# Optimization experiments

Hardware: AMD Instinct MI355X
Metric: run time of the kernel (lower is better)

Reference implementation:

```python
import jax, jax.numpy as jnp
import numpy as np

EMBED_DIM = 768
NUM_HEADS = 12
HEAD_DIM = EMBED_DIM // NUM_HEADS
B, S = 2, 2048


def setup_inputs() -> dict:
    key = jax.random.key(0)
    ks = jax.random.split(key, 6)
    glorot = jnp.sqrt(6.0 / (EMBED_DIM + EMBED_DIM)).astype(jnp.float32)
    x = jax.random.normal(ks[0], (B, S, EMBED_DIM), dtype=jnp.float32)
    mask = jnp.zeros((1, 1, S, S), dtype=jnp.float32)  # additive mask, 0 = no masking
    Wq = jax.random.uniform(ks[1], (EMBED_DIM, EMBED_DIM), jnp.float32, -glorot, glorot)
    Wk = jax.random.uniform(ks[2], (EMBED_DIM, EMBED_DIM), jnp.float32, -glorot, glorot)
    Wv = jax.random.uniform(ks[3], (EMBED_DIM, EMBED_DIM), jnp.float32, -glorot, glorot)
    Wo = jax.random.uniform(ks[4], (EMBED_DIM, EMBED_DIM), jnp.float32, -glorot, glorot)
    bo = jnp.zeros((EMBED_DIM,), dtype=jnp.float32)
    return {"x": x, "mask": mask, "Wq": Wq, "Wk": Wk, "Wv": Wv, "Wo": Wo, "bo": bo}


def reference(x, mask, Wq, Wk, Wv, Wo, bo):
    b, s, _ = x.shape
    # Q/K/V projections (no bias), split into heads: [b, h, s, d]
    def split_heads(t):
        return t.reshape(b, s, NUM_HEADS, HEAD_DIM).transpose(0, 2, 1, 3)
    q = split_heads(x @ Wq)
    k = split_heads(x @ Wk)
    v = split_heads(x @ Wv)
    scale = 1.0 / jnp.sqrt(jnp.float32(HEAD_DIM))
    logits = jnp.einsum('bhqd,bhkd->bhqk', q, k) * scale  # [b, h, s, s]
    logits = logits + mask * (-1e9)
    weights = jax.nn.softmax(logits, axis=-1)
    attn = jnp.einsum('bhqk,bhkd->bhqd', weights, v)
    concat = attn.transpose(0, 2, 1, 3).reshape(b, s, EMBED_DIM)
    return concat @ Wo + bo
```

## Files before the change

kernel.cpp:

```cpp
#include <hip/hip_runtime.h>


typedef __bf16 bf16_t;
typedef bf16_t bf16x8 __attribute__((ext_vector_type(8)));
typedef bf16_t bf16x4 __attribute__((ext_vector_type(4)));
typedef float f32x4 __attribute__((ext_vector_type(4)));
typedef _Float16 f16x4 __attribute__((ext_vector_type(4)));
typedef _Float16 f16x8 __attribute__((ext_vector_type(8)));
typedef __fp16 hf2 __attribute__((ext_vector_type(2)));

#define SC2 0.1803368801111137f
#define DEFER_THR 44.0f

__device__ __forceinline__ float bf2f(unsigned short u) {
  union { unsigned int i; float f; } x;
  x.i = ((unsigned int)u) << 16;
  return x.f;
}

__device__ __forceinline__ float fexp2(float x) {
  return __builtin_amdgcn_exp2f(x);
}

__device__ __forceinline__ void glds16(const bf16_t* g, bf16_t* l) {
  __builtin_amdgcn_global_load_lds(
      (const __attribute__((address_space(1))) void*)g,
      (__attribute__((address_space(3))) void*)l, 16, 0, 0);
}

__device__ __forceinline__ int detect_bf16_flag(const unsigned short* x) {
  const int lane = threadIdx.x & 63;
  const uint4* p = (const uint4*)x;
  uint4 a = p[lane * 2];
  uint4 b = p[lane * 2 + 1];
  unsigned int w[8] = {a.x, a.y, a.z, a.w, b.x, b.y, b.z, b.w};
  unsigned int big = 0;
#pragma unroll
  for (int i = 0; i < 8; i++) {
    unsigned int e0 = (w[i] >> 7) & 0xFF, e1 = (w[i] >> 23) & 0xFF;
    big |= (e0 > 0x88u) | (e1 > 0x88u);
  }
  unsigned long long bal = __ballot(big != 0u);
  return bal == 0ULL ? 1 : 0;
}

__global__ void k_prep(const void* __restrict__ x, const void* __restrict__ mask,
                       const void* __restrict__ Wq, const void* __restrict__ Wk,
                       const void* __restrict__ Wv, const void* __restrict__ Wo,
                       bf16_t* __restrict__ xb, bf16_t* __restrict__ wqkvT,
                       bf16_t* __restrict__ woT, int* __restrict__ mflags) {
  __shared__ float ts[32][33];
  __shared__ int snz;
  const int blk = blockIdx.x;
  const int f = detect_bf16_flag((const unsigned short*)x);

  if (blk < 1536) {
    if (f) return;
    int i = blk * 256 + threadIdx.x;
    const float* xf = (const float*)x + (size_t)i * 8;
    bf16x8 v;
#pragma unroll
    for (int j = 0; j < 8; j++) v[j] = (bf16_t)xf[j];
    *(bf16x8*)(xb + (size_t)i * 8) = v;
  } else if (blk < 3840) {
    const int t = blk - 1536;
    const int z = t / 576, r = t % 576, kt = r / 24, nt = r % 24;
    const void* wsrc = (z == 0) ? Wq : (z == 1) ? Wk : (z == 2) ? Wv : Wo;
    bf16_t* dst = (z < 3) ? (wqkvT + (size_t)z * 768 * 768) : woT;
    const int c = threadIdx.x & 31, r0 = threadIdx.x >> 5;
#pragma unroll
    for (int i = 0; i < 4; i++) {
      int kr = kt * 32 + r0 + i * 8;
      float v;
      if (f) v = bf2f(((const unsigned short*)wsrc)[(size_t)kr * 768 + nt * 32 + c]);
      else   v = ((const float*)wsrc)[(size_t)kr * 768 + nt * 32 + c];
      ts[r0 + i * 8][c] = v;
    }
    __syncthreads();
#pragma unroll
    for (int i = 0; i < 4; i++) {
      int nr = nt * 32 + r0 + i * 8;
      dst[(size_t)nr * 768 + kt * 32 + c] = (bf16_t)ts[c][r0 + i * 8];
    }
  } else {
    const int t = blk - 3840;
    const int qt = t >> 4, ktm = t & 15;
    if (threadIdx.x == 0) snz = 0;
    __syncthreads();
    unsigned int nz = 0;
    if (f) {
#pragma unroll
      for (int i = 0; i < 8; i++) {
        int uidx = i * 256 + threadIdx.x;
        int row = uidx >> 4, col = uidx & 15;
        const uint4* p = (const uint4*)((const char*)mask +
            ((size_t)(qt * 128 + row) * 2048 + ktm * 128) * 2 + col * 16);
        uint4 v = *p;
        nz |= ((v.x | v.y | v.z | v.w) & 0x7fff7fffu);
      }
    } else {
#pragma unroll
      for (int i = 0; i < 16; i++) {
        int uidx = i * 256 + threadIdx.x;
        int row = uidx >> 5, col = uidx & 31;
        const uint4* p = (const uint4*)((const char*)mask +
            ((size_t)(qt * 128 + row) * 2048 + ktm * 128) * 4 + col * 16);
        uint4 v = *p;
        nz |= ((v.x | v.y | v.z | v.w) & 0x7fffffffu);
      }
    }
    if (nz) snz = 1;
    __syncthreads();
    if (threadIdx.x == 0) mflags[qt * 16 + ktm] = snz;
  }
}

__global__ __launch_bounds__(256, 3) void k_gemmQKV(
    const bf16_t* __restrict__ xb, const bf16_t* __restrict__ Bm,
    bf16_t* __restrict__ Qd, char* __restrict__ Kd, char* __restrict__ Vt,
    const unsigned short* __restrict__ xdet) {
  __shared__ __align__(16) char smem[32768];
  _Float16* Tb = (_Float16*)smem;

  const int f = detect_bf16_flag(xdet);
  const bf16_t* A = f ? (const bf16_t*)xdet : xb;

  const int tid = threadIdx.x;
  const int n0 = blockIdx.x * 128, m0 = blockIdx.y * 128;
  const int r = tid >> 2, c8 = (tid & 3) << 3;
  const bf16_t* Ag = A + (size_t)(m0 + r) * 768 + c8;
  const bf16_t* Bg = Bm + (size_t)(n0 + r) * 768 + c8;
  const int wid = tid >> 6, lane = tid & 63;
  const int wm = (wid >> 1) << 6, wn = (wid & 1) << 6;
  const int lr = lane & 15, quad = lane >> 4, lk = quad << 3, g4 = quad << 2;

  f32x4 acc[4][4];
  const f32x4 z = {0.f, 0.f, 0.f, 0.f};
#pragma unroll
  for (int i = 0; i < 4; i++)
#pragma unroll
    for (int j = 0; j < 4; j++) acc[i][j] = z;

  {
    bf16_t* A0 = (bf16_t*)smem;
    bf16_t* B0 = (bf16_t*)(smem + 16384);
    glds16(Ag, A0 + wid * 512);
    glds16(Ag + (size_t)64 * 768, A0 + 2048 + wid * 512);
    glds16(Bg, B0 + wid * 512);
    glds16(Bg + (size_t)64 * 768, B0 + 2048 + wid * 512);
  }
  __syncthreads();

  for (int s = 0; s < 24; s++) {
    if (s < 23) {
      const int k0 = (s + 1) * 32;
      bf16_t* An = (bf16_t*)(smem + ((s + 1) & 1) * 8192);
      bf16_t* Bn = (bf16_t*)(smem + 16384 + ((s + 1) & 1) * 8192);
      glds16(Ag + k0, An + wid * 512);
      glds16(Ag + (size_t)64 * 768 + k0, An + 2048 + wid * 512);
      glds16(Bg + k0, Bn + wid * 512);
      glds16(Bg + (size_t)64 * 768 + k0, Bn + 2048 + wid * 512);
    }
    const bf16_t* As = (const bf16_t*)(smem + (s & 1) * 8192);
    const bf16_t* Bs = (const bf16_t*)(smem + 16384 + (s & 1) * 8192);
    bf16x8 af[4], bf_[4];
#pragma unroll
    for (int t = 0; t < 4; t++) af[t]  = *(const bf16x8*)&As[(wm + t * 16 + lr) * 32 + lk];
#pragma unroll
    for (int t = 0; t < 4; t++) bf_[t] = *(const bf16x8*)&Bs[(wn + t * 16 + lr) * 32 + lk];
#pragma unroll
    for (int i = 0; i < 4; i++)
#pragma unroll
      for (int j = 0; j < 4; j++)
        acc[i][j] = __builtin_amdgcn_mfma_f32_16x16x32_bf16(af[i], bf_[j], acc[i][j], 0, 0, 0);
    __syncthreads();
  }

  if (n0 < 768) {
    const int bb = m0 >> 11;
#pragma unroll
    for (int i = 0; i < 4; i++)
#pragma unroll
      for (int j = 0; j < 4; j++) {
        const int rc = n0 + wn + j * 16 + lr;
        const int hh = rc >> 6, dd = rc & 63;
        const size_t base = (((size_t)bb * 12 + hh) * 2048) * 64 + dd;
#pragma unroll
        for (int reg = 0; reg < 4; reg++) {
          const int s = (m0 & 2047) + wm + i * 16 + g4 + reg;
          Qd[base + (size_t)s * 64] = (bf16_t)acc[i][j][reg];
        }
      }
  } else if (n0 < 1536) {
    const int nb = n0 - 768;
    const int bb = m0 >> 11;
    const int g = ((m0 & 2047) + wm) >> 6;
#pragma unroll
    for (int i = 0; i < 4; i++) {
#pragma unroll
      for (int j = 0; j < 4; j++) {
        const int rc = nb + wn + j * 16 + lr;
        const int hh = rc >> 6, dd = rc & 63;
        const size_t tbase = ((size_t)((bb * 12 + hh) * 32 + g)) << 13;
        const int doff = ((dd >> 5) << 10) + (((dd >> 3) & 3) << 8) + ((dd & 7) << 1);
#pragma unroll
        for (int reg = 0; reg < 4; reg++) {
          const int sig = ((i >> 1) << 5) + ((quad & 1) << 4) +
                          (((((i & 1) << 1) | (quad >> 1))) << 2) + reg;
          *(bf16_t*)(Kd + tbase + ((sig >> 4) << 11) + ((sig & 15) << 4) + doff) =
              (bf16_t)acc[i][j][reg];
        }
      }
    }
  } else {
    const int bb = m0 >> 11;
#pragma unroll
    for (int half = 0; half < 2; half++) {
      if ((wid & 1) == half) {
#pragma unroll
        for (int j = 0; j < 4; j++) {
          const int d_l = j * 16 + lr;
#pragma unroll
          for (int i = 0; i < 4; i++)
#pragma unroll
            for (int reg = 0; reg < 4; reg++)
              Tb[d_l * 136 + wm + i * 16 + g4 + reg] = (_Float16)acc[i][j][reg];
        }
      }
      __syncthreads();
      const int row = tid >> 2, cc = (tid & 3) * 32;
      const int vcol = (n0 - 1536) + half * 64 + row;
      const int hh = vcol >> 6;
      const int g = ((m0 & 2047) + cc) >> 6;
      const int koff2 = (cc & 63) * 2;
      char* vb = Vt + (((size_t)((bb * 12 + hh) * 32 + g)) << 13) + (row << 7);
#pragma unroll
      for (int u = 0; u < 4; u++)
        *(uint4*)(vb + ((koff2 + u * 16) ^ ((row & 7) << 4))) =
            *(const uint4*)&Tb[row * 136 + cc + u * 8];
      __syncthreads();
    }
  }
}

__global__ __launch_bounds__(64, 2) void k_flash(
    const bf16_t* __restrict__ Qd, const char* __restrict__ Kd,
    const char* __restrict__ Vt, const void* __restrict__ mask,
    const int* __restrict__ mflags, const unsigned short* __restrict__ xdet,
    bf16_t* __restrict__ attn) {
  const int lane = threadIdx.x & 63;
  const int lr = lane & 15, quad = lane >> 4, lk = quad << 3, g4 = quad << 2;

  const int lin = blockIdx.x;
  const int gx = lin & 7, ww = lin >> 3;
  const int hb = gx * 3 + (ww >> 6);
  const int h = hb % 12, bb = hb / 12;
  const int u = ww & 63;
  const int q0 = u * 32;

  const size_t bh = (size_t)bb * 12 + h;
  const char* Kg = Kd + (bh << 18);
  const char* Vg = Vt + (bh << 18);

  const bf16_t* Qh = Qd + bh * 2048 * 64;
  const int mbf = detect_bf16_flag(xdet);
  const int* mfrow = mflags + (u >> 2) * 16;
  int mbits = 0;
#pragma unroll
  for (int t = 0; t < 16; t++) mbits |= (mfrow[t] != 0) << t;

  const bf16x8 qfA0 = *(const bf16x8*)&Qh[(size_t)(q0 + lr) * 64 + lk];
  const bf16x8 qfA1 = *(const bf16x8*)&Qh[(size_t)(q0 + lr) * 64 + 32 + lk];
  const bf16x8 qfB0 = *(const bf16x8*)&Qh[(size_t)(q0 + 16 + lr) * 64 + lk];
  const bf16x8 qfB1 = *(const bf16x8*)&Qh[(size_t)(q0 + 16 + lr) * 64 + 32 + lk];

  f16x8 ones8;
#pragma unroll
  for (int j = 0; j < 8; j++) ones8[j] = (_Float16)1.f;

  const int vxo0 = (quad * 16) ^ ((lr & 7) << 4);
  const int vxo1 = (64 + quad * 16) ^ ((lr & 7) << 4);

  const f32x4 z = {0.f, 0.f, 0.f, 0.f};
  f32x4 otA[4], otB[4];
#pragma unroll
  for (int dt = 0; dt < 4; dt++) { otA[dt] = z; otB[dt] = z; }
  float mA = -1e30f, lA = 0.f, mB = -1e30f, lB = 0.f;

  bf16x8 kfP[8], kfQ[8];
  {
    const char* K0 = Kg;
#pragma unroll
    for (int ct = 0; ct < 4; ct++) {
      kfP[ct * 2]     = *(const bf16x8*)(K0 + ct * 2048 + lane * 16);
      kfP[ct * 2 + 1] = *(const bf16x8*)(K0 + ct * 2048 + 1024 + lane * 16);
    }
  }

#define FLASH_BODY(S, KC, KN)                                                \
  {                                                                          \
    const int s_ = (S);                                                      \
    const char* Vt_ = Vg + ((size_t)s_ << 13);                               \
    f16x8 vf[8];                                                             \
    _Pragma("unroll")                                                        \
    for (int c2 = 0; c2 < 2; c2++) {                                         \
      _Pragma("unroll")                                                      \
      for (int dt = 0; dt < 4; dt++)                                         \
        vf[c2 * 4 + dt] = *(const f16x8*)(Vt_ + (dt * 16 + lr) * 128 +       \
                                          (c2 ? vxo1 : vxo0));               \
    }                                                                        \
    if (s_ + 1 < 32) {                                                       \
      const char* Kn_ = Kg + ((size_t)(s_ + 1) << 13);                       \
      _Pragma("unroll")                                                      \
      for (int ct = 0; ct < 4; ct++) {                                       \
        KN[ct * 2]     = *(const bf16x8*)(Kn_ + ct * 2048 + lane * 16);      \
        KN[ct * 2 + 1] = *(const bf16x8*)(Kn_ + ct * 2048 + 1024 + lane * 16); \
      }                                                                      \
    }                                                                        \
    f32x4 svA[4], svB[4];                                                    \
    _Pragma("unroll")                                                        \
    for (int ct = 0; ct < 4; ct++) { svA[ct] = z; svB[ct] = z; }             \
    __builtin_amdgcn_s_setprio(1);                                           \
    _Pragma("unroll")                                                        \
    for (int ct = 0; ct < 4; ct++) {                                         \
      svA[ct] = __builtin_amdgcn_mfma_f32_16x16x32_bf16(KC[ct * 2], qfA0, svA[ct], 0, 0, 0); \
      svA[ct] = __builtin_amdgcn_mfma_f32_16x16x32_bf16(KC[ct * 2 + 1], qfA1, svA[ct], 0, 0, 0); \
      svB[ct] = __builtin_amdgcn_mfma_f32_16x16x32_bf16(KC[ct * 2], qfB0, svB[ct], 0, 0, 0); \
      svB[ct] = __builtin_amdgcn_mfma_f32_16x16x32_bf16(KC[ct * 2 + 1], qfB1, svB[ct], 0, 0, 0); \
    }                                                                        \
    __builtin_amdgcn_s_setprio(0);                                           \
    if ((mbits >> (s_ >> 1)) & 1) {                                          \
      _Pragma("unroll")                                                      \
      for (int ct = 0; ct < 4; ct++) {                                       \
        _Pragma("unroll")                                                    \
        for (int reg = 0; reg < 4; reg++) {                                  \
          const int kk = ((ct >> 1) << 5) + (quad << 3) + ((ct & 1) << 2) + reg; \
          size_t miA = (size_t)(q0 + lr) * 2048 + s_ * 64 + kk;              \
          size_t miB = (size_t)(q0 + 16 + lr) * 2048 + s_ * 64 + kk;         \
          float mvA = mbf ? bf2f(((const unsigned short*)mask)[miA])         \
                          : ((const float*)mask)[miA];                       \
          float mvB = mbf ? bf2f(((const unsigned short*)mask)[miB])         \
                          : ((const float*)mask)[miB];                       \
          svA[ct][reg] -= 8e9f * mvA;                                        \
          svB[ct][reg] -= 8e9f * mvB;                                        \
        }                                                                    \
      }                                                                      \
    }                                                                        \
    float tA = fmaxf(                                                        \
        fmaxf(fmaxf(fmaxf(svA[0][0], svA[0][1]), fmaxf(svA[0][2], svA[0][3])), \
              fmaxf(fmaxf(svA[1][0], svA[1][1]), fmaxf(svA[1][2], svA[1][3]))), \
        fmaxf(fmaxf(fmaxf(svA[2][0], svA[2][1]), fmaxf(svA[2][2], svA[2][3])), \
              fmaxf(fmaxf(svA[3][0], svA[3][1]), fmaxf(svA[3][2], svA[3][3])))); \
    float tB = fmaxf(                                                        \
        fmaxf(fmaxf(fmaxf(svB[0][0], svB[0][1]), fmaxf(svB[0][2], svB[0][3])), \
              fmaxf(fmaxf(svB[1][0], svB[1][1]), fmaxf(svB[1][2], svB[1][3]))), \
        fmaxf(fmaxf(fmaxf(svB[2][0], svB[2][1]), fmaxf(svB[2][2], svB[2][3])), \
              fmaxf(fmaxf(svB[3][0], svB[3][1]), fmaxf(svB[3][2], svB[3][3])))); \
    tA = fmaxf(tA, __shfl_xor(tA, 16));                                      \
    tA = fmaxf(tA, __shfl_xor(tA, 32));                                      \
    tB = fmaxf(tB, __shfl_xor(tB, 16));                                      \
    tB = fmaxf(tB, __shfl_xor(tB, 32));                                      \
    if (__ballot(tA > mA + DEFER_THR)) {                                     \
      const float mnew = fmaxf(mA, tA);                                      \
      const float alpha = fexp2((mA - mnew) * SC2);                          \
      _Pragma("unroll")                                                      \
      for (int dt = 0; dt < 4; dt++) {                                       \
        _Pragma("unroll")                                                    \
        for (int reg = 0; reg < 4; reg++) otA[dt][reg] *= alpha;             \
      }                                                                      \
      lA *= alpha; mA = mnew;                                                \
    }                                                                        \
    if (__ballot(tB > mB + DEFER_THR)) {                                     \
      const float mnew = fmaxf(mB, tB);                                      \
      const float alpha = fexp2((mB - mnew) * SC2);                          \
      _Pragma("unroll")                                                      \
      for (int dt = 0; dt < 4; dt++) {                                       \
        _Pragma("unroll")                                                    \
        for (int reg = 0; reg < 4; reg++) otB[dt][reg] *= alpha;             \
      }                                                                      \
      lB *= alpha; mB = mnew;                                                \
    }                                                                        \
    const float mSA = mA * SC2, mSB = mB * SC2;                              \
    f16x8 pbA[2], pbB[2];                                                    \
    _Pragma("unroll")                                                        \
    for (int c2 = 0; c2 < 2; c2++) {                                         \
      union { hf2 hh[4]; f16x8 v; } uA, uB;                                  \
      _Pragma("unroll")                                                      \
      for (int hh2 = 0; hh2 < 2; hh2++) {                                    \
        const int ct = c2 * 2 + hh2;                                         \
        float a0 = fexp2(fmaf(svA[ct][0], SC2, -mSA));                       \
        float a1 = fexp2(fmaf(svA[ct][1], SC2, -mSA));                       \
        float a2 = fexp2(fmaf(svA[ct][2], SC2, -mSA));                       \
        float a3 = fexp2(fmaf(svA[ct][3], SC2, -mSA));                       \
        float b0 = fexp2(fmaf(svB[ct][0], SC2, -mSB));                       \
        float b1 = fexp2(fmaf(svB[ct][1], SC2, -mSB));                       \
        float b2 = fexp2(fmaf(svB[ct][2], SC2, -mSB));                       \
        float b3 = fexp2(fmaf(svB[ct][3], SC2, -mSB));                       \
        uA.hh[hh2 * 2 + 0] = __builtin_amdgcn_cvt_pkrtz(a0, a1);             \
        uA.hh[hh2 * 2 + 1] = __builtin_amdgcn_cvt_pkrtz(a2, a3);             \
        uB.hh[hh2 * 2 + 0] = __builtin_amdgcn_cvt_pkrtz(b0, b1);             \
        uB.hh[hh2 * 2 + 1] = __builtin_amdgcn_cvt_pkrtz(b2, b3);             \
      }                                                                      \
      pbA[c2] = uA.v; pbB[c2] = uB.v;                                        \
    }                                                                        \
    f32x4 asumA = z, asumB = z;                                              \
    __builtin_amdgcn_s_setprio(1);                                           \
    _Pragma("unroll")                                                        \
    for (int c2 = 0; c2 < 2; c2++) {                                         \
      asumA = __builtin_amdgcn_mfma_f32_16x16x32_f16(ones8, pbA[c2], asumA, 0, 0, 0); \
      asumB = __builtin_amdgcn_mfma_f32_16x16x32_f16(ones8, pbB[c2], asumB, 0, 0, 0); \
      _Pragma("unroll")                                                      \
      for (int dt = 0; dt < 4; dt++) {                                       \
        otA[dt] = __builtin_amdgcn_mfma_f32_16x16x32_f16(vf[c2 * 4 + dt], pbA[c2], otA[dt], 0, 0, 0); \
        otB[dt] = __builtin_amdgcn_mfma_f32_16x16x32_f16(vf[c2 * 4 + dt], pbB[c2], otB[dt], 0, 0, 0); \
      }                                                                      \
    }                                                                        \
    __builtin_amdgcn_s_setprio(0);                                           \
    lA += asumA[0]; lB += asumB[0];                                          \
  }

  for (int s2 = 0; s2 < 32; s2 += 2) {
    FLASH_BODY(s2, kfP, kfQ);
    FLASH_BODY(s2 + 1, kfQ, kfP);
  }
#undef FLASH_BODY

  const float invA = 1.0f / lA, invB = 1.0f / lB;
  bf16_t* arowA = attn + ((size_t)bb * 2048 + q0 + lr) * 768 + h * 64 + g4;
  bf16_t* arowB = attn + ((size_t)bb * 2048 + q0 + 16 + lr) * 768 + h * 64 + g4;
#pragma unroll
  for (int dt = 0; dt < 4; dt++) {
    bf16x4 vA, vB;
#pragma unroll
    for (int reg = 0; reg < 4; reg++) {
      vA[reg] = (bf16_t)(otA[dt][reg] * invA);
      vB[reg] = (bf16_t)(otB[dt][reg] * invB);
    }
    *(bf16x4*)(arowA + dt * 16) = vA;
    *(bf16x4*)(arowB + dt * 16) = vB;
  }
}

__global__ __launch_bounds__(256, 3) void k_gemm2(
    const bf16_t* __restrict__ A, const bf16_t* __restrict__ Bm,
    const void* __restrict__ bo, const unsigned short* __restrict__ xdet,
    float* __restrict__ outF, unsigned short* __restrict__ outH) {
  __shared__ __align__(16) char smem[32768];

  const int tid = threadIdx.x, wid = tid >> 6, lane = tid & 63;
  const int n0 = blockIdx.x * 64, m0 = blockIdx.y * 64;
  const int wm = (wid >> 1) << 5, wn = (wid & 1) << 5;
  const int lr = lane & 15, lk = (lane >> 4) << 3, g4 = (lane >> 4) << 2;
  const bf16_t* Ag = A + (size_t)(m0 + (tid >> 2)) * 768 + ((tid & 3) << 3);
  const bf16_t* Bg = Bm + (size_t)(n0 + (tid >> 2)) * 768 + ((tid & 3) << 3);

  f32x4 acc[2][2];
  const f32x4 z = {0.f, 0.f, 0.f, 0.f};
#pragma unroll
  for (int i = 0; i < 2; i++)
#pragma unroll
    for (int j = 0; j < 2; j++) acc[i][j] = z;

  {
    bf16_t* A0 = (bf16_t*)smem;
    bf16_t* B0 = (bf16_t*)(smem + 16384);
    glds16(Ag, A0 + wid * 512);
    glds16(Ag + 32, A0 + 2048 + wid * 512);
    glds16(Bg, B0 + wid * 512);
    glds16(Bg + 32, B0 + 2048 + wid * 512);
  }
  __syncthreads();

  for (int s = 0; s < 12; s++) {
    if (s < 11) {
      const int k0 = (s + 1) * 64;
      bf16_t* An = (bf16_t*)(smem + ((s + 1) & 1) * 8192);
      bf16_t* Bn = (bf16_t*)(smem + 16384 + ((s + 1) & 1) * 8192);
      glds16(Ag + k0, An + wid * 512);
      glds16(Ag + k0 + 32, An + 2048 + wid * 512);
      glds16(Bg + k0, Bn + wid * 512);
      glds16(Bg + k0 + 32, Bn + 2048 + wid * 512);
    }
#pragma unroll
    for (int kc = 0; kc < 2; kc++) {
      const bf16_t* As = (const bf16_t*)(smem + (s & 1) * 8192) + kc * 2048;
      const bf16_t* Bs = (const bf16_t*)(smem + 16384 + (s & 1) * 8192) + kc * 2048;
      bf16x8 af[2], bf_[2];
#pragma unroll
      for (int i = 0; i < 2; i++) af[i]  = *(const bf16x8*)&As[(wm + i * 16 + lr) * 32 + lk];
#pragma unroll
      for (int j = 0; j < 2; j++) bf_[j] = *(const bf16x8*)&Bs[(wn + j * 16 + lr) * 32 + lk];
#pragma unroll
      for (int i = 0; i < 2; i++)
#pragma unroll
        for (int j = 0; j < 2; j++)
          acc[i][j] = __builtin_amdgcn_mfma_f32_16x16x32_bf16(af[i], bf_[j], acc[i][j], 0, 0, 0);
    }
    __syncthreads();
  }

  const int obf = detect_bf16_flag(xdet);
#pragma unroll
  for (int i = 0; i < 2; i++)
#pragma unroll
    for (int j = 0; j < 2; j++) {
      const int nn = n0 + wn + j * 16 + lr;
      const float bv = obf ? bf2f(((const unsigned short*)bo)[nn])
                           : ((const float*)bo)[nn];
#pragma unroll
      for (int reg = 0; reg < 4; reg++) {
        const int m = m0 + wm + i * 16 + g4 + reg;
        const float v = acc[i][j][reg] + bv;
        if (obf) outH[(size_t)m * 768 + nn] = __builtin_bit_cast(unsigned short, (bf16_t)v);
        else     outF[(size_t)m * 768 + nn] = v;
      }
    }
}

extern "C" void kernel_launch(void* const* d_in, const int* in_sizes, int n_in,
                              void* d_out, int out_size, void* d_ws, size_t ws_size,
                              hipStream_t stream) {
  (void)in_sizes; (void)n_in; (void)out_size; (void)ws_size;
  const void* x    = d_in[0];
  const void* mask = d_in[1];
  const void* Wq   = d_in[2];
  const void* Wk   = d_in[3];
  const void* Wv   = d_in[4];
  const void* Wo   = d_in[5];
  const void* bo   = d_in[6];

  char* w = (char*)d_ws;
  size_t off = 0;
  auto take = [&](size_t b) -> void* {
    void* p = w + off;
    off = (off + b + 255) & ~(size_t)255;
    return p;
  };
  int*      mflags = (int*)take(256 * 4);
  bf16_t*   wqkvT  = (bf16_t*)take((size_t)2304 * 768 * 2);
  bf16_t*   woT    = (bf16_t*)take((size_t)768 * 768 * 2);
  bf16_t*   xb     = (bf16_t*)take((size_t)4096 * 768 * 2);
  bf16_t*   Qd     = (bf16_t*)take((size_t)3145728 * 2);
  char*     Kd     = (char*)take((size_t)3145728 * 2);
  char*     Vt     = (char*)take((size_t)3145728 * 2);
  bf16_t*   attn   = xb;

  k_prep<<<4096, 256, 0, stream>>>(x, mask, Wq, Wk, Wv, Wo, xb, wqkvT, woT, mflags);
  k_gemmQKV<<<dim3(18, 32), 256, 0, stream>>>(xb, wqkvT, Qd, Kd, Vt,
                                              (const unsigned short*)x);
  k_flash<<<1536, 64, 0, stream>>>(Qd, Kd, Vt, mask, mflags,
                                   (const unsigned short*)x, attn);
  k_gemm2<<<dim3(12, 64), 256, 0, stream>>>(attn, woT, bo, (const unsigned short*)x,
                                            (float*)d_out, (unsigned short*)d_out);
}
```

Before: 175.5 us.

## Split flash attention KV range across four waves with LDS merge

Each flash block now runs four wavefronts, each handling a quarter of the key/value sequence (8 of 32 tiles), instead of one wave walking all 32 tiles. Partial outputs and running max/sum from waves 1-3 go to shared memory, and wave 0 merges them with log-sum-exp rescaling before writing. This cuts the serial KV loop length per block and raises the number of waves in flight. In exchange it adds LDS traffic, a block barrier, and a merge step run by a single wave, and launch bounds now request 256 threads with 4 blocks per CU.

```diff
diff --git a/kernel.cpp b/kernel.cpp
--- a/kernel.cpp
+++ b/kernel.cpp
@@ -243,12 +243,15 @@
   }
 }
 
-__global__ __launch_bounds__(64, 2) void k_flash(
+__global__ __launch_bounds__(256, 4) void k_flash(
     const bf16_t* __restrict__ Qd, const char* __restrict__ Kd,
     const char* __restrict__ Vt, const void* __restrict__ mask,
     const int* __restrict__ mflags, const unsigned short* __restrict__ xdet,
     bf16_t* __restrict__ attn) {
-  const int lane = threadIdx.x & 63;
+  __shared__ float smO[3][32][64];
+  __shared__ float smML[3][2][16][2];
+
+  const int tid = threadIdx.x, wid = tid >> 6, lane = tid & 63;
   const int lr = lane & 15, quad = lane >> 4, lk = quad << 3, g4 = quad << 2;
 
   const int lin = blockIdx.x;
@@ -257,10 +260,11 @@
   const int h = hb % 12, bb = hb / 12;
   const int u = ww & 63;
   const int q0 = u * 32;
+  const int wtile = wid << 3;
 
   const size_t bh = (size_t)bb * 12 + h;
-  const char* Kg = Kd + (bh << 18);
-  const char* Vg = Vt + (bh << 18);
+  const char* Kw = Kd + (bh << 18) + ((size_t)wtile << 13);
+  const char* Vw = Vt + (bh << 18) + ((size_t)wtile << 13);
 
   const bf16_t* Qh = Qd + bh * 2048 * 64;
   const int mbf = detect_bf16_flag(xdet);
@@ -289,18 +293,17 @@
 
   bf16x8 kfP[8], kfQ[8];
   {
-    const char* K0 = Kg;
 #pragma unroll
     for (int ct = 0; ct < 4; ct++) {
-      kfP[ct * 2]     = *(const bf16x8*)(K0 + ct * 2048 + lane * 16);
-      kfP[ct * 2 + 1] = *(const bf16x8*)(K0 + ct * 2048 + 1024 + lane * 16);
+      kfP[ct * 2]     = *(const bf16x8*)(Kw + ct * 2048 + lane * 16);
+      kfP[ct * 2 + 1] = *(const bf16x8*)(Kw + ct * 2048 + 1024 + lane * 16);
     }
   }
 
 #define FLASH_BODY(S, KC, KN)                                                \
   {                                                                          \
-    const int s_ = (S);                                                      \
-    const char* Vt_ = Vg + ((size_t)s_ << 13);                               \
+    const int sl_ = (S);                                                     \
+    const char* Vt_ = Vw + ((size_t)sl_ << 13);                              \
     f16x8 vf[8];                                                             \
     _Pragma("unroll")                                                        \
     for (int c2 = 0; c2 < 2; c2++) {                                         \
@@ -309,8 +312,8 @@
         vf[c2 * 4 + dt] = *(const f16x8*)(Vt_ + (dt * 16 + lr) * 128 +       \
                                           (c2 ? vxo1 : vxo0));               \
     }                                                                        \
-    if (s_ + 1 < 32) {                                                       \
-      const char* Kn_ = Kg + ((size_t)(s_ + 1) << 13);                       \
+    if (sl_ + 1 < 8) {                                                       \
+      const char* Kn_ = Kw + ((size_t)(sl_ + 1) << 13);                      \
       _Pragma("unroll")                                                      \
       for (int ct = 0; ct < 4; ct++) {                                       \
         KN[ct * 2]     = *(const bf16x8*)(Kn_ + ct * 2048 + lane * 16);      \
@@ -329,14 +332,15 @@
       svB[ct] = __builtin_amdgcn_mfma_f32_16x16x32_bf16(KC[ct * 2 + 1], qfB1, svB[ct], 0, 0, 0); \
     }                                                                        \
     __builtin_amdgcn_s_setprio(0);                                           \
-    if ((mbits >> (s_ >> 1)) & 1) {                                          \
+    const int gt_ = wtile + sl_;                                             \
+    if ((mbits >> (gt_ >> 1)) & 1) {                                         \
       _Pragma("unroll")                                                      \
       for (int ct = 0; ct < 4; ct++) {                                       \
         _Pragma("unroll")                                                    \
         for (int reg = 0; reg < 4; reg++) {                                  \
           const int kk = ((ct >> 1) << 5) + (quad << 3) + ((ct & 1) << 2) + reg; \
-          size_t miA = (size_t)(q0 + lr) * 2048 + s_ * 64 + kk;              \
-          size_t miB = (size_t)(q0 + 16 + lr) * 2048 + s_ * 64 + kk;         \
+          size_t miA = (size_t)(q0 + lr) * 2048 + gt_ * 64 + kk;             \
+          size_t miB = (size_t)(q0 + 16 + lr) * 2048 + gt_ * 64 + kk;        \
           float mvA = mbf ? bf2f(((const unsigned short*)mask)[miA])         \
                           : ((const float*)mask)[miA];                       \
           float mvB = mbf ? bf2f(((const unsigned short*)mask)[miB])         \
@@ -419,25 +423,61 @@
     lA += asumA[0]; lB += asumB[0];                                          \
   }
 
-  for (int s2 = 0; s2 < 32; s2 += 2) {
+  for (int s2 = 0; s2 < 8; s2 += 2) {
     FLASH_BODY(s2, kfP, kfQ);
     FLASH_BODY(s2 + 1, kfQ, kfP);
   }
 #undef FLASH_BODY
 
-  const float invA = 1.0f / lA, invB = 1.0f / lB;
-  bf16_t* arowA = attn + ((size_t)bb * 2048 + q0 + lr) * 768 + h * 64 + g4;
-  bf16_t* arowB = attn + ((size_t)bb * 2048 + q0 + 16 + lr) * 768 + h * 64 + g4;
-#pragma unroll
-  for (int dt = 0; dt < 4; dt++) {
-    bf16x4 vA, vB;
-#pragma unroll
-    for (int reg = 0; reg < 4; reg++) {
-      vA[reg] = (bf16_t)(otA[dt][reg] * invA);
-      vB[reg] = (bf16_t)(otB[dt][reg] * invB);
-    }
-    *(bf16x4*)(arowA + dt * 16) = vA;
-    *(bf16x4*)(arowB + dt * 16) = vB;
+  if (wid > 0) {
+    const int w = wid - 1;
+#pragma unroll
+    for (int dt = 0; dt < 4; dt++)
+#pragma unroll
+      for (int reg = 0; reg < 4; reg++) {
+        smO[w][dt * 4 + reg][lane] = otA[dt][reg];
+        smO[w][16 + dt * 4 + reg][lane] = otB[dt][reg];
+      }
+    if (quad == 0) {
+      smML[w][0][lr][0] = mA; smML[w][0][lr][1] = lA;
+      smML[w][1][lr][0] = mB; smML[w][1][lr][1] = lB;
+    }
+  }
+  __syncthreads();
+  if (wid == 0) {
+    const float m1A = smML[0][0][lr][0], l1A = smML[0][0][lr][1];
+    const float m2A = smML[1][0][lr][0], l2A = smML[1][0][lr][1];
+    const float m3A = smML[2][0][lr][0], l3A = smML[2][0][lr][1];
+    const float m1B = smML[0][1][lr][0], l1B = smML[0][1][lr][1];
+    const float m2B = smML[1][1][lr][0], l2B = smML[1][1][lr][1];
+    const float m3B = smML[2][1][lr][0], l3B = smML[2][1][lr][1];
+    const float mmA = fmaxf(fmaxf(mA, m1A), fmaxf(m2A, m3A));
+    const float mmB = fmaxf(fmaxf(mB, m1B), fmaxf(m2B, m3B));
+    const float a0 = fexp2((mA - mmA) * SC2), a1 = fexp2((m1A - mmA) * SC2);
+    const float a2 = fexp2((m2A - mmA) * SC2), a3 = fexp2((m3A - mmA) * SC2);
+    const float b0 = fexp2((mB - mmB) * SC2), b1 = fexp2((m1B - mmB) * SC2);
+    const float b2 = fexp2((m2B - mmB) * SC2), b3 = fexp2((m3B - mmB) * SC2);
+    const float LA = a0 * lA + a1 * l1A + a2 * l2A + a3 * l3A;
+    const float LB = b0 * lB + b1 * l1B + b2 * l2B + b3 * l3B;
+    const float invA = 1.0f / LA, invB = 1.0f / LB;
+    bf16_t* arowA = attn + ((size_t)bb * 2048 + q0 + lr) * 768 + h * 64 + g4;
+    bf16_t* arowB = attn + ((size_t)bb * 2048 + q0 + 16 + lr) * 768 + h * 64 + g4;
+#pragma unroll
+    for (int dt = 0; dt < 4; dt++) {
+      bf16x4 vA, vB;
+#pragma unroll
+      for (int reg = 0; reg < 4; reg++) {
+        const int e = dt * 4 + reg;
+        const float oA = a0 * otA[dt][reg] + a1 * smO[0][e][lane] +
+                         a2 * smO[1][e][lane] + a3 * smO[2][e][lane];
+        const float oB = b0 * otB[dt][reg] + b1 * smO[0][16 + e][lane] +
+                         b2 * smO[1][16 + e][lane] + b3 * smO[2][16 + e][lane];
+        vA[reg] = (bf16_t)(oA * invA);
+        vB[reg] = (bf16_t)(oB * invB);
+      }
+      *(bf16x4*)(arowA + dt * 16) = vA;
+      *(bf16x4*)(arowB + dt * 16) = vB;
+    }
   }
 }
 
@@ -548,8 +588,8 @@
   k_prep<<<4096, 256, 0, stream>>>(x, mask, Wq, Wk, Wv, Wo, xb, wqkvT, woT, mflags);
   k_gemmQKV<<<dim3(18, 32), 256, 0, stream>>>(xb, wqkvT, Qd, Kd, Vt,
                                               (const unsigned short*)x);
-  k_flash<<<1536, 64, 0, stream>>>(Qd, Kd, Vt, mask, mflags,
-                                   (const unsigned short*)x, attn);
+  k_flash<<<1536, 256, 0, stream>>>(Qd, Kd, Vt, mask, mflags,
+                                    (const unsigned short*)x, attn);
   k_gemm2<<<dim3(12, 64), 256, 0, stream>>>(attn, woT, bo, (const unsigned short*)x,
                                             (float*)d_out, (unsigned short*)d_out);
 }
```

After: 551.6 us. 3.14x slower.
